# Performance work log

Hardware: AMD Instinct MI355X
Metric: run time of the kernel (lower is better)

The kernel has to match this reference:

```python
import jax, jax.numpy as jnp
import numpy as np

N = 100000      # num_entities
D = 128         # embedding_dim
H = 128         # hidden_layer_size
R2 = 100        # num_relations * 2 (with inverse relations)
B = 4           # num_bases
E = 400000      # num_edges


def setup_inputs() -> dict:
    key = jax.random.key(0)
    ks = jax.random.split(key, 12)
    s = 0.1
    return {
        "edge_index": jax.random.randint(ks[0], (2, E), 0, N),
        "edge_type": jax.random.randint(ks[1], (E,), 0, R2),
        "entity_embedding": jax.random.normal(ks[2], (N, D), jnp.float32) * s,
        "entity_embedding_bias": jnp.zeros((1, D), jnp.float32),
        "bases1": jax.random.normal(ks[3], (B, D, H), jnp.float32) * s,
        "comp1": jax.random.normal(ks[4], (R2, B), jnp.float32) * s,
        "root1": jax.random.normal(ks[5], (D, H), jnp.float32) * s,
        "bias1": jnp.zeros((H,), jnp.float32),
        "bases2": jax.random.normal(ks[6], (B, H, D), jnp.float32) * s,
        "comp2": jax.random.normal(ks[7], (R2, B), jnp.float32) * s,
        "root2": jax.random.normal(ks[8], (H, D), jnp.float32) * s,
        "bias2": jnp.zeros((D,), jnp.float32),
        "rel_emb": jax.random.normal(ks[9], (R2, D), jnp.float32) * s,
    }


def _rgcn_layer(x, bases, comp, root, bias, src, dst, et, norm):
    # gather source features and project through all bases: [E, B, out]
    xb = jnp.einsum('ei,bio->ebo', x[src], bases)
    # relation-specific basis mix per edge: [E, out]
    msg = jnp.einsum('eb,ebo->eo', comp[et], xb) * norm[:, None]
    # scatter-add aggregate to destination nodes
    agg = jax.ops.segment_sum(msg, dst, num_segments=N)
    return agg + x @ root + bias


def reference(edge_index, edge_type, entity_embedding, entity_embedding_bias,
              bases1, comp1, root1, bias1, bases2, comp2, root2, bias2, rel_emb):
    src, dst = edge_index[0], edge_index[1]
    # schlichtkrull normalization: 1 / |{edges into dst with same relation}|
    key = dst * R2 + edge_type
    counts = jax.ops.segment_sum(jnp.ones((E,), jnp.float32), key, num_segments=N * R2)
    norm = 1.0 / jnp.maximum(counts[key], 1.0)

    x = jax.nn.relu(entity_embedding + entity_embedding_bias)
    x = _rgcn_layer(x, bases1, comp1, root1, bias1, src, dst, edge_type, norm)
    x = jax.nn.relu(x)
    x = _rgcn_layer(x, bases2, comp2, root2, bias2, src, dst, edge_type, norm)

    # DistMult decoder over triples (src, edge_type, dst)
    score = jnp.sum(x[src] * rel_emb[edge_type] * x[dst], axis=-1)  # [E]
    # L2 penalty on relation embeddings
    penalty = jnp.sum(rel_emb ** 2)
    return score, penalty
```

## Files before the change

### kernel.cpp

```cpp
#include <hip/hip_runtime.h>

#define N_NODES 100000
#define DIM     128
#define RR      100
#define NE      400000
#define NBLK    196
#define NPB     32

typedef float  floatx4 __attribute__((ext_vector_type(4)));
typedef __bf16 bf16x8  __attribute__((ext_vector_type(8)));

static __device__ __forceinline__ unsigned short f2b(float f) {
    union { float f; unsigned int i; } v; v.f = f;
    unsigned int u = v.i;
    unsigned int r = (u + 0x7fffu + ((u >> 16) & 1u)) >> 16;
    return (unsigned short)r;
}
static __device__ __forceinline__ float b2f(unsigned int u16) {
    union { unsigned int i; float f; } v; v.i = u16 << 16; return v.f;
}
static __device__ __forceinline__ unsigned packbf(float a, float b) {
    return (unsigned)f2b(a) | ((unsigned)f2b(b) << 16);
}

__global__ void k_deg(const int* __restrict__ dst, int* __restrict__ deg, int E) {
    int e = blockIdx.x * 256 + threadIdx.x;
    if (e < E) atomicAdd(&deg[dst[e]], 1);
}

__global__ void k_scan_block(const int* __restrict__ deg, int* __restrict__ bsum) {
    __shared__ int sm[256];
    int b = blockIdx.x, t = threadIdx.x;
    int i0 = b * 512 + 2 * t;
    int a = (i0     < N_NODES) ? deg[i0]     : 0;
    int c = (i0 + 1 < N_NODES) ? deg[i0 + 1] : 0;
    sm[t] = a + c;
    __syncthreads();
    for (int s = 128; s > 0; s >>= 1) { if (t < s) sm[t] += sm[t + s]; __syncthreads(); }
    if (t == 0) bsum[b] = sm[0];
}

__global__ void k_scan_top(const int* __restrict__ bsum, int* __restrict__ boff) {
    __shared__ int sm[256];
    int t = threadIdx.x;
    int v = (t < NBLK) ? bsum[t] : 0;
    sm[t] = v;
    __syncthreads();
    for (int s = 1; s < 256; s <<= 1) {
        int u = (t >= s) ? sm[t - s] : 0;
        __syncthreads();
        sm[t] += u;
        __syncthreads();
    }
    if (t < NBLK) boff[t] = sm[t] - v;
}

__global__ void k_scan_down(const int* __restrict__ deg, const int* __restrict__ boff,
                            int* __restrict__ off) {
    __shared__ int sm[256];
    int b = blockIdx.x, t = threadIdx.x;
    int i0 = b * 512 + 2 * t;
    int a = (i0     < N_NODES) ? deg[i0]     : 0;
    int c = (i0 + 1 < N_NODES) ? deg[i0 + 1] : 0;
    int ts = a + c;
    sm[t] = ts;
    __syncthreads();
    for (int s = 1; s < 256; s <<= 1) {
        int u = (t >= s) ? sm[t - s] : 0;
        __syncthreads();
        sm[t] += u;
        __syncthreads();
    }
    int base = boff[b] + (sm[t] - ts);
    if (i0     < N_NODES) off[i0]     = base;
    if (i0 + 1 < N_NODES) off[i0 + 1] = base + a;
    if (b == 0 && t == 0) off[N_NODES] = NE;
}

__global__ void k_scatter(const int* __restrict__ src, const int* __restrict__ dst,
                          const int* __restrict__ et, const int* __restrict__ off,
                          int* __restrict__ cursor, int4* __restrict__ edesc, int E) {
    int e = blockIdx.x * 256 + threadIdx.x;
    if (e >= E) return;
    int d = dst[e];
    int pos = off[d] + atomicAdd(&cursor[d], 1);
    edesc[pos] = make_int4(src[e], et[e], d, 0);
}

__global__ void k_norm2(const int* __restrict__ off, int4* __restrict__ edesc, int E) {
    int p = blockIdx.x * 256 + threadIdx.x;
    if (p >= E) return;
    int4 me = edesc[p];
    int p0 = off[me.z], p1 = off[me.z + 1];
    int c = 0;
    for (int j = p0; j < p1; ++j)
        c += (((const int*)edesc)[4 * j + 1] == me.y) ? 1 : 0;
    ((int*)edesc)[4 * p + 3] = __float_as_int(1.0f / (float)c);
}

__global__ void k_pre(const float* __restrict__ ent, const float* __restrict__ entb,
                      const float* __restrict__ bases1, const float* __restrict__ root1,
                      const float* __restrict__ bases2, const float* __restrict__ root2,
                      const float* __restrict__ rel,
                      unsigned short* __restrict__ x1,
                      unsigned short* __restrict__ wt1, unsigned short* __restrict__ wt2,
                      unsigned short* __restrict__ relb, float* __restrict__ out) {
    int b = blockIdx.x, t = threadIdx.x;
    if (b < 50000) {
        int i = b * 256 + t;
        float v = ent[i] + entb[i & (DIM - 1)];
        x1[i] = f2b(v > 0.0f ? v : 0.0f);
    } else if (b < 50320) {
        int i = (b - 50000) * 256 + t;
        int m = i / 640, k = i - m * 640;
        float v1, v2;
        if (k < 512) {
            int bb = k >> 7, kin = k & 127;
            v1 = bases1[(bb * 128 + kin) * 128 + m];
            v2 = bases2[(bb * 128 + kin) * 128 + m];
        } else {
            int kin = k - 512;
            v1 = root1[kin * 128 + m];
            v2 = root2[kin * 128 + m];
        }
        wt1[i] = f2b(v1);
        wt2[i] = f2b(v2);
    } else if (b < 50370) {
        int i = (b - 50320) * 256 + t;
        relb[i] = f2b(rel[i]);
    } else {
        __shared__ float sm[256];
        float v = 0.0f;
        for (int i = t; i < RR * DIM; i += 256) { float x = rel[i]; v += x * x; }
        sm[t] = v;
        __syncthreads();
        for (int s = 128; s > 0; s >>= 1) {
            if (t < s) sm[t] += sm[t + s];
            __syncthreads();
        }
        if (t == 0) out[NE] = sm[0];
    }
}

#define ACC(A) { A[0].x += w0 * xv0; A[0].y += w0 * xv1; \
                 A[1].x += w1 * xv0; A[1].y += w1 * xv1; \
                 A[2].x += w2 * xv0; A[2].y += w2 * xv1; \
                 A[3].x += w3 * xv0; A[3].y += w3 * xv1; }

__global__ __launch_bounds__(512, 4) void k_fused(const unsigned short* __restrict__ X,
                                                  const int4* __restrict__ edesc,
                                                  const int* __restrict__ off,
                                                  const float* __restrict__ comp,
                                                  const unsigned short* __restrict__ WT,
                                                  const float* __restrict__ bias,
                                                  unsigned short* __restrict__ out,
                                                  int do_relu) {
    __shared__ __align__(16) unsigned short Sacc[4 * NPB * 128];
    __shared__ __align__(16) unsigned short Bs[128 * 128];
    __shared__ float4 Cs[RR];

    const int t = threadIdx.x, wid = t >> 6, lane = t & 63;
    const int rbase = blockIdx.x * NPB;

    if (t < RR) Cs[t] = ((const float4*)comp)[t];
    __syncthreads();

    {
        const int nbase = rbase + wid * 4;
        const int lo = off[nbase], hi = off[nbase + 4];
        float2 a0[4], a1[4], a2[4], a3[4];
#pragma unroll
        for (int c = 0; c < 4; ++c) {
            a0[c] = make_float2(0.f, 0.f); a1[c] = make_float2(0.f, 0.f);
            a2[c] = make_float2(0.f, 0.f); a3[c] = make_float2(0.f, 0.f);
        }
        for (int base = lo; base < hi; base += 16) {
            int cnt = hi - base; if (cnt > 16) cnt = 16;
            int4 md = edesc[base + (lane & 15)];
            unsigned xp[16];
#pragma unroll
            for (int u = 0; u < 16; ++u) {
                int jc = (u < cnt) ? u : 0;
                int s = (int)__builtin_amdgcn_readlane((unsigned)md.x, (unsigned)jc);
                xp[u] = *(const unsigned*)(X + (size_t)s * 128 + 2 * lane);
            }
#pragma unroll
            for (int u = 0; u < 16; ++u) {
                if (u < cnt) {
                    int row = (int)__builtin_amdgcn_readlane((unsigned)md.z, (unsigned)u) - nbase;
                    int tt  = (int)__builtin_amdgcn_readlane((unsigned)md.y, (unsigned)u);
                    float w = __int_as_float(__builtin_amdgcn_readlane((unsigned)md.w, (unsigned)u));
                    float4 cc = Cs[tt];
                    float xv0 = b2f(xp[u] & 0xffffu), xv1 = b2f(xp[u] >> 16);
                    float w0 = w * cc.x, w1 = w * cc.y, w2 = w * cc.z, w3 = w * cc.w;
                    if      (row == 0) ACC(a0)
                    else if (row == 1) ACC(a1)
                    else if (row == 2) ACC(a2)
                    else               ACC(a3)
                }
            }
        }
        const int sw16 = lane >> 2, wo = 2 * (lane & 3);
#pragma unroll
        for (int r = 0; r < 4; ++r) {
            int R = wid * 4 + r;
            unsigned bo = (unsigned)(R * 128 + ((sw16 ^ (R & 15)) << 3) + wo);
            float2* A = (r == 0) ? a0 : (r == 1) ? a1 : (r == 2) ? a2 : a3;
#pragma unroll
            for (int c = 0; c < 4; ++c)
                *(unsigned*)(Sacc + c * (NPB * 128) + bo) = packbf(A[c].x, A[c].y);
        }
    }

    const int quad = lane >> 4, lr = lane & 15;
    const int wr = wid & 1, wc = wid >> 1;

    bf16x8 ax[4];
    {
        int grow = rbase + wr * 16 + lr;
#pragma unroll
        for (int ks = 0; ks < 4; ++ks)
            ax[ks] = *(const bf16x8*)(X + (size_t)grow * 128 + ks * 32 + quad * 8);
    }

    floatx4 acc[2];
    acc[0] = (floatx4)0.0f; acc[1] = (floatx4)0.0f;

#pragma unroll
    for (int kc = 0; kc < 5; ++kc) {
        __syncthreads();
#pragma unroll
        for (int i = 0; i < 4; ++i) {
            int idx = i * 512 + t;
            int row = idx >> 4, ch = idx & 15;
            uint4 w = *(const uint4*)(WT + (size_t)row * 640 + kc * 128 + ch * 8);
            *(uint4*)(Bs + row * 128 + ((ch ^ (row & 15)) << 3)) = w;
        }
        __syncthreads();
#pragma unroll
        for (int ks = 0; ks < 4; ++ks) {
            bf16x8 a, b0, b1;
            int R = wr * 16 + lr;
            if (kc < 4) {
                int ch = ((ks * 4 + quad) ^ (R & 15)) << 3;
                a = *(const bf16x8*)(Sacc + kc * (NPB * 128) + R * 128 + ch);
            } else {
                a = ax[ks];
            }
            int sch = ((ks * 4 + quad) ^ lr) << 3;
            b0 = *(const bf16x8*)(Bs + (wc * 32 + lr) * 128 + sch);
            b1 = *(const bf16x8*)(Bs + (wc * 32 + 16 + lr) * 128 + sch);
            acc[0] = __builtin_amdgcn_mfma_f32_16x16x32_bf16(a, b0, acc[0], 0, 0, 0);
            acc[1] = __builtin_amdgcn_mfma_f32_16x16x32_bf16(a, b1, acc[1], 0, 0, 0);
        }
    }

#pragma unroll
    for (int reg = 0; reg < 4; ++reg) {
        int R = wr * 16 + quad * 4 + reg;
        int grow = rbase + R;
#pragma unroll
        for (int nj = 0; nj < 2; ++nj) {
            int n = wc * 32 + nj * 16 + lr;
            float v = acc[nj][reg] + bias[n];
            if (do_relu) v = v > 0.0f ? v : 0.0f;
            out[(size_t)grow * 128 + n] = f2b(v);
        }
    }
}

__global__ __launch_bounds__(256) void k_score(const unsigned short* __restrict__ xf,
                                               const int* __restrict__ src, const int* __restrict__ dst,
                                               const int* __restrict__ et,
                                               const unsigned short* __restrict__ relb,
                                               float* __restrict__ out, int E) {
    int g = threadIdx.x >> 4, li = threadIdx.x & 15;
    int e = blockIdx.x * 16 + g;
    if (e >= E) return;
    int s = src[e], d = dst[e], tt = et[e];
    uint4 au = *(const uint4*)(xf + (size_t)s * 128 + li * 8);
    uint4 bu = *(const uint4*)(xf + (size_t)d * 128 + li * 8);
    uint4 ru = *(const uint4*)(relb + (size_t)tt * 128 + li * 8);
    float v;
    v  = b2f(au.x & 0xffffu) * b2f(ru.x & 0xffffu) * b2f(bu.x & 0xffffu);
    v += b2f(au.x >> 16)     * b2f(ru.x >> 16)     * b2f(bu.x >> 16);
    v += b2f(au.y & 0xffffu) * b2f(ru.y & 0xffffu) * b2f(bu.y & 0xffffu);
    v += b2f(au.y >> 16)     * b2f(ru.y >> 16)     * b2f(bu.y >> 16);
    v += b2f(au.z & 0xffffu) * b2f(ru.z & 0xffffu) * b2f(bu.z & 0xffffu);
    v += b2f(au.z >> 16)     * b2f(ru.z >> 16)     * b2f(bu.z >> 16);
    v += b2f(au.w & 0xffffu) * b2f(ru.w & 0xffffu) * b2f(bu.w & 0xffffu);
    v += b2f(au.w >> 16)     * b2f(ru.w >> 16)     * b2f(bu.w >> 16);
    v += __shfl_xor(v, 8, 16);
    v += __shfl_xor(v, 4, 16);
    v += __shfl_xor(v, 2, 16);
    v += __shfl_xor(v, 1, 16);
    if (li == 0) out[e] = v;
}

extern "C" void kernel_launch(void* const* d_in, const int* in_sizes, int n_in,
                              void* d_out, int out_size, void* d_ws, size_t ws_size,
                              hipStream_t stream) {
    (void)in_sizes; (void)n_in; (void)out_size; (void)ws_size;
    const int* edge_index = (const int*)d_in[0];
    const int* edge_type  = (const int*)d_in[1];
    const float* ent    = (const float*)d_in[2];
    const float* entb   = (const float*)d_in[3];
    const float* bases1 = (const float*)d_in[4];
    const float* comp1  = (const float*)d_in[5];
    const float* root1  = (const float*)d_in[6];
    const float* bias1  = (const float*)d_in[7];
    const float* bases2 = (const float*)d_in[8];
    const float* comp2  = (const float*)d_in[9];
    const float* root2  = (const float*)d_in[10];
    const float* bias2  = (const float*)d_in[11];
    const float* rel    = (const float*)d_in[12];
    const int* src = edge_index;
    const int* dst = edge_index + NE;

    char* ws = (char*)d_ws;
    size_t off_b = 0;
    auto alloc = [&](size_t bytes) { void* p = ws + off_b; off_b = (off_b + bytes + 255) & ~(size_t)255; return p; };

    unsigned short* x1   = (unsigned short*)alloc((size_t)N_NODES * 128 * 2);
    unsigned short* x2   = (unsigned short*)alloc((size_t)N_NODES * 128 * 2);
    unsigned short* wt1  = (unsigned short*)alloc(128 * 640 * 2);
    unsigned short* wt2  = (unsigned short*)alloc(128 * 640 * 2);
    unsigned short* relb = (unsigned short*)alloc(RR * DIM * 2);
    int*   deg    = (int*)alloc((size_t)N_NODES * 4);
    int*   cursor = (int*)alloc((size_t)N_NODES * 4);
    int*   offv   = (int*)alloc((size_t)(N_NODES + 1) * 4);
    int*   bsum   = (int*)alloc(NBLK * 4);
    int*   boff   = (int*)alloc(NBLK * 4);
    int4*  edesc  = (int4*)alloc((size_t)(NE + 64) * 16);

    float* out = (float*)d_out;

    hipMemsetAsync(deg, 0, (size_t)N_NODES * 4, stream);
    hipMemsetAsync(cursor, 0, (size_t)N_NODES * 4, stream);

    k_deg<<<(NE + 255) / 256, 256, 0, stream>>>(dst, deg, NE);
    k_scan_block<<<NBLK, 256, 0, stream>>>(deg, bsum);
    k_scan_top<<<1, 256, 0, stream>>>(bsum, boff);
    k_scan_down<<<NBLK, 256, 0, stream>>>(deg, boff, offv);
    k_scatter<<<(NE + 255) / 256, 256, 0, stream>>>(src, dst, edge_type, offv, cursor, edesc, NE);
    k_norm2<<<(NE + 255) / 256, 256, 0, stream>>>(offv, edesc, NE);
    k_pre<<<50371, 256, 0, stream>>>(ent, entb, bases1, root1, bases2, root2, rel,
                                     x1, wt1, wt2, relb, out);

    int fgrid = N_NODES / NPB;
    k_fused<<<fgrid, 512, 0, stream>>>(x1, edesc, offv, comp1, wt1, bias1, x2, 1);
    k_fused<<<fgrid, 512, 0, stream>>>(x2, edesc, offv, comp2, wt2, bias2, x1, 0);
    k_score<<<(NE + 15) / 16, 256, 0, stream>>>(x1, src, dst, edge_type, relb, out, NE);
}
```

Baseline: 400.1 us.

## Score edges grouped by destination via CSR and pack edge id into descriptor

The DistMult score kernel now walks the dst-sorted CSR edge list, one wavefront per destination node. It loads the destination feature row once and reuses it across all incoming edges, instead of gathering it separately per edge. To write results back in the original order, the edge index is packed into the type field of the edge descriptor, which changes the decode in the norm and fused kernels. The aggregation accumulators also switch to two-wide float vectors, which may allow packed FMA. The cost is load imbalance across nodes with different degrees and scattered output writes.

Result: no change. 406.1 us (+1.5%).

```diff
diff --git a/kernel.cpp b/kernel.cpp
--- a/kernel.cpp
+++ b/kernel.cpp
@@ -8,6 +8,7 @@
 #define NPB     32
 
 typedef float  floatx4 __attribute__((ext_vector_type(4)));
+typedef float  floatx2 __attribute__((ext_vector_type(2)));
 typedef __bf16 bf16x8  __attribute__((ext_vector_type(8)));
 
 static __device__ __forceinline__ unsigned short f2b(float f) {
@@ -84,17 +85,18 @@
     if (e >= E) return;
     int d = dst[e];
     int pos = off[d] + atomicAdd(&cursor[d], 1);
-    edesc[pos] = make_int4(src[e], et[e], d, 0);
+    edesc[pos] = make_int4(src[e], (et[e] << 19) | e, d, 0);
 }
 
 __global__ void k_norm2(const int* __restrict__ off, int4* __restrict__ edesc, int E) {
     int p = blockIdx.x * 256 + threadIdx.x;
     if (p >= E) return;
     int4 me = edesc[p];
+    int myt = me.y >> 19;
     int p0 = off[me.z], p1 = off[me.z + 1];
     int c = 0;
     for (int j = p0; j < p1; ++j)
-        c += (((const int*)edesc)[4 * j + 1] == me.y) ? 1 : 0;
+        c += ((((const int*)edesc)[4 * j + 1] >> 19) == myt) ? 1 : 0;
     ((int*)edesc)[4 * p + 3] = __float_as_int(1.0f / (float)c);
 }
 
@@ -142,10 +144,10 @@
     }
 }
 
-#define ACC(A) { A[0].x += w0 * xv0; A[0].y += w0 * xv1; \
-                 A[1].x += w1 * xv0; A[1].y += w1 * xv1; \
-                 A[2].x += w2 * xv0; A[2].y += w2 * xv1; \
-                 A[3].x += w3 * xv0; A[3].y += w3 * xv1; }
+#define ACC(A) { A[0] += (floatx2){w0, w0} * xv; \
+                 A[1] += (floatx2){w1, w1} * xv; \
+                 A[2] += (floatx2){w2, w2} * xv; \
+                 A[3] += (floatx2){w3, w3} * xv; }
 
 __global__ __launch_bounds__(512, 4) void k_fused(const unsigned short* __restrict__ X,
                                                   const int4* __restrict__ edesc,
@@ -168,11 +170,11 @@
     {
         const int nbase = rbase + wid * 4;
         const int lo = off[nbase], hi = off[nbase + 4];
-        float2 a0[4], a1[4], a2[4], a3[4];
+        floatx2 a0[4], a1[4], a2[4], a3[4];
 #pragma unroll
         for (int c = 0; c < 4; ++c) {
-            a0[c] = make_float2(0.f, 0.f); a1[c] = make_float2(0.f, 0.f);
-            a2[c] = make_float2(0.f, 0.f); a3[c] = make_float2(0.f, 0.f);
+            a0[c] = (floatx2)0.0f; a1[c] = (floatx2)0.0f;
+            a2[c] = (floatx2)0.0f; a3[c] = (floatx2)0.0f;
         }
         for (int base = lo; base < hi; base += 16) {
             int cnt = hi - base; if (cnt > 16) cnt = 16;
@@ -188,10 +190,10 @@
             for (int u = 0; u < 16; ++u) {
                 if (u < cnt) {
                     int row = (int)__builtin_amdgcn_readlane((unsigned)md.z, (unsigned)u) - nbase;
-                    int tt  = (int)__builtin_amdgcn_readlane((unsigned)md.y, (unsigned)u);
+                    int tt  = (int)__builtin_amdgcn_readlane((unsigned)md.y, (unsigned)u) >> 19;
                     float w = __int_as_float(__builtin_amdgcn_readlane((unsigned)md.w, (unsigned)u));
                     float4 cc = Cs[tt];
-                    float xv0 = b2f(xp[u] & 0xffffu), xv1 = b2f(xp[u] >> 16);
+                    floatx2 xv = {b2f(xp[u] & 0xffffu), b2f(xp[u] >> 16)};
                     float w0 = w * cc.x, w1 = w * cc.y, w2 = w * cc.z, w3 = w * cc.w;
                     if      (row == 0) ACC(a0)
                     else if (row == 1) ACC(a1)
@@ -205,7 +207,7 @@
         for (int r = 0; r < 4; ++r) {
             int R = wid * 4 + r;
             unsigned bo = (unsigned)(R * 128 + ((sw16 ^ (R & 15)) << 3) + wo);
-            float2* A = (r == 0) ? a0 : (r == 1) ? a1 : (r == 2) ? a2 : a3;
+            floatx2* A = (r == 0) ? a0 : (r == 1) ? a1 : (r == 2) ? a2 : a3;
 #pragma unroll
             for (int c = 0; c < 4; ++c)
                 *(unsigned*)(Sacc + c * (NPB * 128) + bo) = packbf(A[c].x, A[c].y);
@@ -270,31 +272,42 @@
 }
 
 __global__ __launch_bounds__(256) void k_score(const unsigned short* __restrict__ xf,
-                                               const int* __restrict__ src, const int* __restrict__ dst,
-                                               const int* __restrict__ et,
+                                               const int4* __restrict__ edesc,
+                                               const int* __restrict__ off,
                                                const unsigned short* __restrict__ relb,
-                                               float* __restrict__ out, int E) {
-    int g = threadIdx.x >> 4, li = threadIdx.x & 15;
-    int e = blockIdx.x * 16 + g;
-    if (e >= E) return;
-    int s = src[e], d = dst[e], tt = et[e];
-    uint4 au = *(const uint4*)(xf + (size_t)s * 128 + li * 8);
+                                               float* __restrict__ out) {
+    int wid = threadIdx.x >> 6, lane = threadIdx.x & 63;
+    int d = blockIdx.x * 4 + wid;
+    if (d >= N_NODES) return;
+    int p0 = off[d], p1 = off[d + 1];
+    if (p0 == p1) return;
+    int g = lane >> 4, li = lane & 15;
     uint4 bu = *(const uint4*)(xf + (size_t)d * 128 + li * 8);
-    uint4 ru = *(const uint4*)(relb + (size_t)tt * 128 + li * 8);
-    float v;
-    v  = b2f(au.x & 0xffffu) * b2f(ru.x & 0xffffu) * b2f(bu.x & 0xffffu);
-    v += b2f(au.x >> 16)     * b2f(ru.x >> 16)     * b2f(bu.x >> 16);
-    v += b2f(au.y & 0xffffu) * b2f(ru.y & 0xffffu) * b2f(bu.y & 0xffffu);
-    v += b2f(au.y >> 16)     * b2f(ru.y >> 16)     * b2f(bu.y >> 16);
-    v += b2f(au.z & 0xffffu) * b2f(ru.z & 0xffffu) * b2f(bu.z & 0xffffu);
-    v += b2f(au.z >> 16)     * b2f(ru.z >> 16)     * b2f(bu.z >> 16);
-    v += b2f(au.w & 0xffffu) * b2f(ru.w & 0xffffu) * b2f(bu.w & 0xffffu);
-    v += b2f(au.w >> 16)     * b2f(ru.w >> 16)     * b2f(bu.w >> 16);
-    v += __shfl_xor(v, 8, 16);
-    v += __shfl_xor(v, 4, 16);
-    v += __shfl_xor(v, 2, 16);
-    v += __shfl_xor(v, 1, 16);
-    if (li == 0) out[e] = v;
+    float bf0 = b2f(bu.x & 0xffffu), bf1 = b2f(bu.x >> 16);
+    float bf2 = b2f(bu.y & 0xffffu), bf3 = b2f(bu.y >> 16);
+    float bf4 = b2f(bu.z & 0xffffu), bf5 = b2f(bu.z >> 16);
+    float bf6 = b2f(bu.w & 0xffffu), bf7 = b2f(bu.w >> 16);
+    for (int p = p0 + g; p < p1; p += 4) {
+        int4 e = edesc[p];
+        int et = e.y >> 19;
+        int eidx = e.y & 0x7FFFF;
+        uint4 au = *(const uint4*)(xf + (size_t)e.x * 128 + li * 8);
+        uint4 ru = *(const uint4*)(relb + (size_t)et * 128 + li * 8);
+        float v;
+        v  = b2f(au.x & 0xffffu) * b2f(ru.x & 0xffffu) * bf0;
+        v += b2f(au.x >> 16)     * b2f(ru.x >> 16)     * bf1;
+        v += b2f(au.y & 0xffffu) * b2f(ru.y & 0xffffu) * bf2;
+        v += b2f(au.y >> 16)     * b2f(ru.y >> 16)     * bf3;
+        v += b2f(au.z & 0xffffu) * b2f(ru.z & 0xffffu) * bf4;
+        v += b2f(au.z >> 16)     * b2f(ru.z >> 16)     * bf5;
+        v += b2f(au.w & 0xffffu) * b2f(ru.w & 0xffffu) * bf6;
+        v += b2f(au.w >> 16)     * b2f(ru.w >> 16)     * bf7;
+        v += __shfl_xor(v, 8, 16);
+        v += __shfl_xor(v, 4, 16);
+        v += __shfl_xor(v, 2, 16);
+        v += __shfl_xor(v, 1, 16);
+        if (li == 0) out[eidx] = v;
+    }
 }
 
 extern "C" void kernel_launch(void* const* d_in, const int* in_sizes, int n_in,
@@ -350,5 +363,5 @@
     int fgrid = N_NODES / NPB;
     k_fused<<<fgrid, 512, 0, stream>>>(x1, edesc, offv, comp1, wt1, bias1, x2, 1);
     k_fused<<<fgrid, 512, 0, stream>>>(x2, edesc, offv, comp2, wt2, bias2, x1, 0);
-    k_score<<<(NE + 15) / 16, 256, 0, stream>>>(x1, src, dst, edge_type, relb, out, NE);
-}
+    k_score<<<(N_NODES + 3) / 4, 256, 0, stream>>>(x1, edesc, offv, relb, out);
+}
```

## Fold zero-init into prep kernel, prefetch weight tiles into registers, pack edge id

Applied to the files above, without the earlier changes.

Removes the two memset calls by zeroing deg and cursor inside k_pre, which now runs first. In the fused RGCN kernel, weight-chunk global loads are prefetched into registers one chunk ahead, so they overlap the MFMA work and the gather phase. The self-row X loads are also hoisted ahead of the gather. Accumulation is written with 2-wide float vectors to encourage packed FMA. Edge type is packed with the edge index into one descriptor field, which adds a shift per read and assumes E < 2^19.

Measured after the change: 592.5 us. 1.48x slower.

```diff
diff --git a/kernel.cpp b/kernel.cpp
--- a/kernel.cpp
+++ b/kernel.cpp
@@ -8,6 +8,7 @@
 #define NPB     32
 
 typedef float  floatx4 __attribute__((ext_vector_type(4)));
+typedef float  floatx2 __attribute__((ext_vector_type(2)));
 typedef __bf16 bf16x8  __attribute__((ext_vector_type(8)));
 
 static __device__ __forceinline__ unsigned short f2b(float f) {
@@ -84,17 +85,18 @@
     if (e >= E) return;
     int d = dst[e];
     int pos = off[d] + atomicAdd(&cursor[d], 1);
-    edesc[pos] = make_int4(src[e], et[e], d, 0);
+    edesc[pos] = make_int4(src[e], (et[e] << 19) | e, d, 0);
 }
 
 __global__ void k_norm2(const int* __restrict__ off, int4* __restrict__ edesc, int E) {
     int p = blockIdx.x * 256 + threadIdx.x;
     if (p >= E) return;
     int4 me = edesc[p];
+    int myt = me.y >> 19;
     int p0 = off[me.z], p1 = off[me.z + 1];
     int c = 0;
     for (int j = p0; j < p1; ++j)
-        c += (((const int*)edesc)[4 * j + 1] == me.y) ? 1 : 0;
+        c += ((((const int*)edesc)[4 * j + 1] >> 19) == myt) ? 1 : 0;
     ((int*)edesc)[4 * p + 3] = __float_as_int(1.0f / (float)c);
 }
 
@@ -104,7 +106,8 @@
                       const float* __restrict__ rel,
                       unsigned short* __restrict__ x1,
                       unsigned short* __restrict__ wt1, unsigned short* __restrict__ wt2,
-                      unsigned short* __restrict__ relb, float* __restrict__ out) {
+                      unsigned short* __restrict__ relb, float* __restrict__ out,
+                      int* __restrict__ deg, int* __restrict__ cursor) {
     int b = blockIdx.x, t = threadIdx.x;
     if (b < 50000) {
         int i = b * 256 + t;
@@ -128,6 +131,10 @@
     } else if (b < 50370) {
         int i = (b - 50320) * 256 + t;
         relb[i] = f2b(rel[i]);
+    } else if (b < 51152) {
+        int j = (b - 50370) * 256 + t;
+        if (j < N_NODES) deg[j] = 0;
+        else if (j < 2 * N_NODES) cursor[j - N_NODES] = 0;
     } else {
         __shared__ float sm[256];
         float v = 0.0f;
@@ -142,10 +149,10 @@
     }
 }
 
-#define ACC(A) { A[0].x += w0 * xv0; A[0].y += w0 * xv1; \
-                 A[1].x += w1 * xv0; A[1].y += w1 * xv1; \
-                 A[2].x += w2 * xv0; A[2].y += w2 * xv1; \
-                 A[3].x += w3 * xv0; A[3].y += w3 * xv1; }
+#define ACC(A) { A[0] += (floatx2){w0, w0} * xv; \
+                 A[1] += (floatx2){w1, w1} * xv; \
+                 A[2] += (floatx2){w2, w2} * xv; \
+                 A[3] += (floatx2){w3, w3} * xv; }
 
 __global__ __launch_bounds__(512, 4) void k_fused(const unsigned short* __restrict__ X,
                                                   const int4* __restrict__ edesc,
@@ -161,6 +168,21 @@
 
     const int t = threadIdx.x, wid = t >> 6, lane = t & 63;
     const int rbase = blockIdx.x * NPB;
+    const int quad = lane >> 4, lr = lane & 15;
+    const int wr = wid & 1, wc = wid >> 1;
+
+    uint4 breg[4];
+    const int srow = t >> 4, sch = t & 15;
+#pragma unroll
+    for (int i = 0; i < 4; ++i)
+        breg[i] = *(const uint4*)(WT + (size_t)(srow + i * 32) * 640 + sch * 8);
+    bf16x8 ax[4];
+    {
+        int grow = rbase + wr * 16 + lr;
+#pragma unroll
+        for (int ks = 0; ks < 4; ++ks)
+            ax[ks] = *(const bf16x8*)(X + (size_t)grow * 128 + ks * 32 + quad * 8);
+    }
 
     if (t < RR) Cs[t] = ((const float4*)comp)[t];
     __syncthreads();
@@ -168,11 +190,11 @@
     {
         const int nbase = rbase + wid * 4;
         const int lo = off[nbase], hi = off[nbase + 4];
-        float2 a0[4], a1[4], a2[4], a3[4];
+        floatx2 a0[4], a1[4], a2[4], a3[4];
 #pragma unroll
         for (int c = 0; c < 4; ++c) {
-            a0[c] = make_float2(0.f, 0.f); a1[c] = make_float2(0.f, 0.f);
-            a2[c] = make_float2(0.f, 0.f); a3[c] = make_float2(0.f, 0.f);
+            a0[c] = (floatx2)0.0f; a1[c] = (floatx2)0.0f;
+            a2[c] = (floatx2)0.0f; a3[c] = (floatx2)0.0f;
         }
         for (int base = lo; base < hi; base += 16) {
             int cnt = hi - base; if (cnt > 16) cnt = 16;
@@ -188,10 +210,10 @@
             for (int u = 0; u < 16; ++u) {
                 if (u < cnt) {
                     int row = (int)__builtin_amdgcn_readlane((unsigned)md.z, (unsigned)u) - nbase;
-                    int tt  = (int)__builtin_amdgcn_readlane((unsigned)md.y, (unsigned)u);
+                    int tt  = (int)__builtin_amdgcn_readlane((unsigned)md.y, (unsigned)u) >> 19;
                     float w = __int_as_float(__builtin_amdgcn_readlane((unsigned)md.w, (unsigned)u));
                     float4 cc = Cs[tt];
-                    float xv0 = b2f(xp[u] & 0xffffu), xv1 = b2f(xp[u] >> 16);
+                    floatx2 xv = {b2f(xp[u] & 0xffffu), b2f(xp[u] >> 16)};
                     float w0 = w * cc.x, w1 = w * cc.y, w2 = w * cc.z, w3 = w * cc.w;
                     if      (row == 0) ACC(a0)
                     else if (row == 1) ACC(a1)
@@ -205,24 +227,13 @@
         for (int r = 0; r < 4; ++r) {
             int R = wid * 4 + r;
             unsigned bo = (unsigned)(R * 128 + ((sw16 ^ (R & 15)) << 3) + wo);
-            float2* A = (r == 0) ? a0 : (r == 1) ? a1 : (r == 2) ? a2 : a3;
+            floatx2* A = (r == 0) ? a0 : (r == 1) ? a1 : (r == 2) ? a2 : a3;
 #pragma unroll
             for (int c = 0; c < 4; ++c)
                 *(unsigned*)(Sacc + c * (NPB * 128) + bo) = packbf(A[c].x, A[c].y);
         }
     }
 
-    const int quad = lane >> 4, lr = lane & 15;
-    const int wr = wid & 1, wc = wid >> 1;
-
-    bf16x8 ax[4];
-    {
-        int grow = rbase + wr * 16 + lr;
-#pragma unroll
-        for (int ks = 0; ks < 4; ++ks)
-            ax[ks] = *(const bf16x8*)(X + (size_t)grow * 128 + ks * 32 + quad * 8);
-    }
-
     floatx4 acc[2];
     acc[0] = (floatx4)0.0f; acc[1] = (floatx4)0.0f;
 
@@ -230,11 +241,12 @@
     for (int kc = 0; kc < 5; ++kc) {
         __syncthreads();
 #pragma unroll
-        for (int i = 0; i < 4; ++i) {
-            int idx = i * 512 + t;
-            int row = idx >> 4, ch = idx & 15;
-            uint4 w = *(const uint4*)(WT + (size_t)row * 640 + kc * 128 + ch * 8);
-            *(uint4*)(Bs + row * 128 + ((ch ^ (row & 15)) << 3)) = w;
+        for (int i = 0; i < 4; ++i)
+            *(uint4*)(Bs + (srow + i * 32) * 128 + ((sch ^ ((srow + i * 32) & 15)) << 3)) = breg[i];
+        if (kc < 4) {
+#pragma unroll
+            for (int i = 0; i < 4; ++i)
+                breg[i] = *(const uint4*)(WT + (size_t)(srow + i * 32) * 640 + (kc + 1) * 128 + sch * 8);
         }
         __syncthreads();
 #pragma unroll
@@ -247,9 +259,9 @@
             } else {
                 a = ax[ks];
             }
-            int sch = ((ks * 4 + quad) ^ lr) << 3;
-            b0 = *(const bf16x8*)(Bs + (wc * 32 + lr) * 128 + sch);
-            b1 = *(const bf16x8*)(Bs + (wc * 32 + 16 + lr) * 128 + sch);
+            int bch = ((ks * 4 + quad) ^ lr) << 3;
+            b0 = *(const bf16x8*)(Bs + (wc * 32 + lr) * 128 + bch);
+            b1 = *(const bf16x8*)(Bs + (wc * 32 + 16 + lr) * 128 + bch);
             acc[0] = __builtin_amdgcn_mfma_f32_16x16x32_bf16(a, b0, acc[0], 0, 0, 0);
             acc[1] = __builtin_amdgcn_mfma_f32_16x16x32_bf16(a, b1, acc[1], 0, 0, 0);
         }
@@ -335,17 +347,14 @@
 
     float* out = (float*)d_out;
 
-    hipMemsetAsync(deg, 0, (size_t)N_NODES * 4, stream);
-    hipMemsetAsync(cursor, 0, (size_t)N_NODES * 4, stream);
-
+    k_pre<<<51153, 256, 0, stream>>>(ent, entb, bases1, root1, bases2, root2, rel,
+                                     x1, wt1, wt2, relb, out, deg, cursor);
     k_deg<<<(NE + 255) / 256, 256, 0, stream>>>(dst, deg, NE);
     k_scan_block<<<NBLK, 256, 0, stream>>>(deg, bsum);
     k_scan_top<<<1, 256, 0, stream>>>(bsum, boff);
     k_scan_down<<<NBLK, 256, 0, stream>>>(deg, boff, offv);
     k_scatter<<<(NE + 255) / 256, 256, 0, stream>>>(src, dst, edge_type, offv, cursor, edesc, NE);
     k_norm2<<<(NE + 255) / 256, 256, 0, stream>>>(offv, edesc, NE);
-    k_pre<<<50371, 256, 0, stream>>>(ent, entb, bases1, root1, bases2, root2, rel,
-                                     x1, wt1, wt2, relb, out);
 
     int fgrid = N_NODES / NPB;
     k_fused<<<fgrid, 512, 0, stream>>>(x1, edesc, offv, comp1, wt1, bias1, x2, 1);
```
